# Optimization experiments

Measured on AMD Instinct MI355X. Metric: run time of the kernel, lower is better.

Reference implementation:

```python
import jax, jax.numpy as jnp
import numpy as np

B, N, F_IN, H, D = 16384, 64, 128, 4, 32


def setup_inputs() -> dict:
    key = jax.random.key(0)
    k1, k2, k3, k4, k5 = jax.random.split(key, 5)
    node_features = jax.random.normal(k1, (B, F_IN), dtype=jnp.float32)
    neighbor_features = jax.random.normal(k2, (B, N, F_IN), dtype=jnp.float32)
    mask = jax.random.randint(k3, (B, N), 0, 2).astype(jnp.bool_)
    # guarantee at least one valid neighbor per row (avoid all -inf softmax)
    neighbor_mask = mask.at[:, 0].set(True)
    # xavier_uniform with gain=1.414
    lim_W = 1.414 * np.sqrt(6.0 / (F_IN + H * D))
    W = jax.random.uniform(k4, (F_IN, H * D), minval=-lim_W, maxval=lim_W, dtype=jnp.float32)
    lim_a = 1.414 * np.sqrt(6.0 / (2 * D + 1))
    a = jax.random.uniform(k5, (H, 2 * D, 1), minval=-lim_a, maxval=lim_a, dtype=jnp.float32)
    return {"node_features": node_features, "neighbor_features": neighbor_features,
            "neighbor_mask": neighbor_mask, "W": W, "a": a}


def reference(node_features, neighbor_features, neighbor_mask, W, a):
    b, n, f_in = neighbor_features.shape
    h, two_d, _ = a.shape
    d = two_d // 2
    # project: (b,h,d) and (b,n,h,d)
    h_node = (node_features @ W).reshape(b, h, d)
    h_nb = (neighbor_features @ W).reshape(b, n, h, d)
    # concat-based additive attention: cat([h_node, h_nb]) @ a == h_node@a1 + h_nb@a2
    a1 = a[:, :d, 0]   # (h, d) node half
    a2 = a[:, d:, 0]   # (h, d) neighbor half
    e = (jnp.einsum('bhd,hd->bh', h_node, a1)[:, None, :]
         + jnp.einsum('bnhd,hd->bnh', h_nb, a2))          # (b, n, h)
    e = jax.nn.leaky_relu(e, negative_slope=0.2)
    e = jnp.where(neighbor_mask[:, :, None], e, -jnp.inf)
    alpha = jax.nn.softmax(e, axis=1)                      # softmax over neighbors
    # dropout is identity in eval mode
    out = jnp.einsum('bnh,bnhd->bhd', alpha, h_nb).reshape(b, h * d)
    return out
```

## Files before the change

### kernel.cpp

```cpp
#include <hip/hip_runtime.h>
#include <cstdint>


typedef __attribute__((ext_vector_type(8))) short bf16x8;
typedef __attribute__((ext_vector_type(4))) float f32x4;

union U16B { uint4 u; bf16x8 f; };

__device__ inline unsigned short f2bf(float x) {
  unsigned int u = __float_as_uint(x);
  unsigned int r = u + 0x7FFFu + ((u >> 16) & 1u);
  return (unsigned short)(r >> 16);
}

__global__ void gat_prep(const float* __restrict__ W, const float* __restrict__ a,
                         unsigned short* __restrict__ Wt, float* __restrict__ wa1) {
  int t = threadIdx.x;
  int blk = blockIdx.x;
  if (blk < 64) {
    int g = blk * 256 + t;
    int c = g >> 7, k = g & 127;
    Wt[c * 128 + k] = f2bf(W[k * 128 + c]);
  } else {
    for (int i = t; i < 512; i += 256) {
      int k = i >> 2, h = i & 3;
      float s = 0.f;
      #pragma unroll
      for (int d = 0; d < 32; ++d) s += W[k * 128 + h * 32 + d] * a[h * 64 + d];
      wa1[i] = s;
    }
  }
}

__global__ __launch_bounds__(256, 4) void gat_main(
    const float* __restrict__ node, const float* __restrict__ nbr,
    const unsigned char* __restrict__ mask, const unsigned short* __restrict__ Wt,
    const float* __restrict__ wa1, const float* __restrict__ a,
    float* __restrict__ out) {
  const int b    = blockIdx.x;
  const int tid  = threadIdx.x;
  const int w    = tid >> 6;
  const int lane = tid & 63;
  const int grp  = lane >> 4;
  const int l15  = lane & 15;

  __shared__ unsigned short Albs[64 * 128];

  unsigned int probe = ((const unsigned int*)mask)[lane];
  bool isByte = (__ballot(probe > 1u) != 0ull);

  bf16x8 bfr[2][4];
  #pragma unroll
  for (int j = 0; j < 2; ++j) {
    #pragma unroll
    for (int ks = 0; ks < 4; ++ks) {
      int c  = (2 * w + j) * 16 + l15;
      int k0 = grp * 8 + ks * 32;
      U16B u; u.u = *(const uint4*)(Wt + c * 128 + k0);
      bfr[j][ks] = u.f;
    }
  }

  float a2lo = a[w * 64 + 32 + l15];
  float a2hi = a[w * 64 + 48 + l15];

  float es = node[b * 128 + lane]      * wa1[lane * 4 + w]
           + node[b * 128 + 64 + lane] * wa1[(64 + lane) * 4 + w];
  #pragma unroll
  for (int m = 32; m >= 1; m >>= 1) es += __shfl_xor(es, m);

  unsigned int okm[4];
  if (isByte) {
    #pragma unroll
    for (int mt = 0; mt < 4; ++mt) {
      unsigned int mb = *(const unsigned int*)(mask + b * 64 + mt * 16 + grp * 4);
      okm[mt] = ((mb & 0xffu)       ? 1u : 0u) |
                ((mb & 0xff00u)     ? 2u : 0u) |
                ((mb & 0xff0000u)   ? 4u : 0u) |
                ((mb & 0xff000000u) ? 8u : 0u);
    }
  } else {
    const uint4* mi = (const uint4*)((const unsigned int*)mask + b * 64);
    #pragma unroll
    for (int mt = 0; mt < 4; ++mt) {
      uint4 mm = mi[mt * 4 + grp];
      okm[mt] = (mm.x ? 1u : 0u) | (mm.y ? 2u : 0u) | (mm.z ? 4u : 0u) | (mm.w ? 8u : 0u);
    }
  }

  {
    const float4* src = (const float4*)(nbr + (size_t)b * 8192);
    #pragma unroll
    for (int rep = 0; rep < 8; ++rep) {
      int v = rep * 256 + tid;
      float4 f = src[v];
      int r  = v >> 5;
      int kb = (v & 31) * 8;
      uint2 p;
      p.x = (unsigned int)f2bf(f.x) | ((unsigned int)f2bf(f.y) << 16);
      p.y = (unsigned int)f2bf(f.z) | ((unsigned int)f2bf(f.w) << 16);
      int byteaddr = (r * 256 + kb) ^ ((r & 7) << 4);
      *(uint2*)((char*)Albs + byteaddr) = p;
    }
  }
  __syncthreads();

  f32x4 acc[4][2];
  #pragma unroll
  for (int mt = 0; mt < 4; ++mt) { acc[mt][0] = f32x4{0,0,0,0}; acc[mt][1] = f32x4{0,0,0,0}; }
  #pragma unroll
  for (int mt = 0; mt < 4; ++mt) {
    #pragma unroll
    for (int ks = 0; ks < 4; ++ks) {
      int r     = mt * 16 + l15;
      int kbyte = (grp * 8 + ks * 32) * 2;
      int addr  = (r * 256 + kbyte) ^ ((r & 7) << 4);
      U16B u; u.u = *(const uint4*)((const char*)Albs + addr);
      acc[mt][0] = __builtin_amdgcn_mfma_f32_16x16x32_bf16(u.f, bfr[0][ks], acc[mt][0], 0, 0, 0);
      acc[mt][1] = __builtin_amdgcn_mfma_f32_16x16x32_bf16(u.f, bfr[1][ks], acc[mt][1], 0, 0, 0);
    }
  }

  float e[4][4];
  #pragma unroll
  for (int mt = 0; mt < 4; ++mt) {
    #pragma unroll
    for (int rg = 0; rg < 4; ++rg) {
      float v = acc[mt][0][rg] * a2lo + acc[mt][1][rg] * a2hi;
      v += __shfl_xor(v, 1); v += __shfl_xor(v, 2);
      v += __shfl_xor(v, 4); v += __shfl_xor(v, 8);
      float s = es + v;
      s = s > 0.f ? s : 0.2f * s;
      bool ok = (okm[mt] >> rg) & 1u;
      e[mt][rg] = ok ? s : -__builtin_inff();
    }
  }

  float M = -__builtin_inff();
  #pragma unroll
  for (int mt = 0; mt < 4; ++mt)
    #pragma unroll
    for (int rg = 0; rg < 4; ++rg) M = fmaxf(M, e[mt][rg]);
  M = fmaxf(M, __shfl_xor(M, 16));
  M = fmaxf(M, __shfl_xor(M, 32));

  float S = 0.f;
  float al[4][4];
  #pragma unroll
  for (int mt = 0; mt < 4; ++mt) {
    #pragma unroll
    for (int rg = 0; rg < 4; ++rg) {
      float p = __expf(e[mt][rg] - M);
      al[mt][rg] = p;
      S += p;
    }
  }
  S += __shfl_xor(S, 16);
  S += __shfl_xor(S, 32);
  float inv = 1.f / S;

  float po0 = 0.f, po1 = 0.f;
  #pragma unroll
  for (int mt = 0; mt < 4; ++mt) {
    #pragma unroll
    for (int rg = 0; rg < 4; ++rg) {
      po0 += al[mt][rg] * acc[mt][0][rg];
      po1 += al[mt][rg] * acc[mt][1][rg];
    }
  }
  po0 += __shfl_xor(po0, 16); po0 += __shfl_xor(po0, 32);
  po1 += __shfl_xor(po1, 16); po1 += __shfl_xor(po1, 32);
  po0 *= inv; po1 *= inv;

  if (lane < 32) {
    float vOut = (lane & 16) ? po1 : po0;
    out[b * 128 + w * 32 + lane] = vOut;
  }
}

extern "C" void kernel_launch(void* const* d_in, const int* in_sizes, int n_in,
                              void* d_out, int out_size, void* d_ws, size_t ws_size,
                              hipStream_t stream) {
  (void)in_sizes; (void)n_in; (void)out_size; (void)ws_size;
  const float* node = (const float*)d_in[0];
  const float* nbr  = (const float*)d_in[1];
  const unsigned char* mask = (const unsigned char*)d_in[2];
  const float* W    = (const float*)d_in[3];
  const float* a    = (const float*)d_in[4];
  float* out = (float*)d_out;

  unsigned short* Wt = (unsigned short*)d_ws;
  float* wa1 = (float*)((char*)d_ws + 32768);

  gat_prep<<<65, 256, 0, stream>>>(W, a, Wt, wa1);
  gat_main<<<16384, 256, 0, stream>>>(node, nbr, mask, Wt, wa1, a, out);
}
```

Baseline: 696.6 us.

## Process two batch rows per block with double-buffered LDS staging

Each block now handles two batch rows, so the block count is halved. The W fragment loads, a2 and wa1 loads are shared across both rows. The second row's neighbor tile is issued into registers before the first sync and written to a second LDS buffer while the first row is computed, overlapping global loads with MFMA work. LDS use per block doubles to 32 KB, register pressure rises from holding the 8 float4s, and launch bounds drop from 4 to 3 blocks per CU.

```diff
diff --git a/kernel.cpp b/kernel.cpp
--- a/kernel.cpp
+++ b/kernel.cpp
@@ -32,19 +32,97 @@
   }
 }
 
-__global__ __launch_bounds__(256, 4) void gat_main(
+__device__ __forceinline__ void compute_node(
+    const char* __restrict__ Abase, const bf16x8 (&bfr)[2][4],
+    float a2lo, float a2hi, float es, const unsigned int (&okm)[4],
+    int lane, int grp, int l15, int w, float* __restrict__ outp) {
+  f32x4 acc[4][2];
+  #pragma unroll
+  for (int mt = 0; mt < 4; ++mt) { acc[mt][0] = f32x4{0,0,0,0}; acc[mt][1] = f32x4{0,0,0,0}; }
+  #pragma unroll
+  for (int mt = 0; mt < 4; ++mt) {
+    #pragma unroll
+    for (int ks = 0; ks < 4; ++ks) {
+      int r     = mt * 16 + l15;
+      int kbyte = (grp * 8 + ks * 32) * 2;
+      int addr  = (r * 256 + kbyte) ^ ((r & 7) << 4);
+      U16B u; u.u = *(const uint4*)(Abase + addr);
+      acc[mt][0] = __builtin_amdgcn_mfma_f32_16x16x32_bf16(u.f, bfr[0][ks], acc[mt][0], 0, 0, 0);
+      acc[mt][1] = __builtin_amdgcn_mfma_f32_16x16x32_bf16(u.f, bfr[1][ks], acc[mt][1], 0, 0, 0);
+    }
+  }
+
+  float e[4][4];
+  #pragma unroll
+  for (int mt = 0; mt < 4; ++mt) {
+    #pragma unroll
+    for (int rg = 0; rg < 4; ++rg) {
+      float v = acc[mt][0][rg] * a2lo + acc[mt][1][rg] * a2hi;
+      v += __shfl_xor(v, 1); v += __shfl_xor(v, 2);
+      v += __shfl_xor(v, 4); v += __shfl_xor(v, 8);
+      float s = es + v;
+      s = s > 0.f ? s : 0.2f * s;
+      bool ok = (okm[mt] >> rg) & 1u;
+      e[mt][rg] = ok ? s : -__builtin_inff();
+    }
+  }
+
+  float M = -__builtin_inff();
+  #pragma unroll
+  for (int mt = 0; mt < 4; ++mt)
+    #pragma unroll
+    for (int rg = 0; rg < 4; ++rg) M = fmaxf(M, e[mt][rg]);
+  M = fmaxf(M, __shfl_xor(M, 16));
+  M = fmaxf(M, __shfl_xor(M, 32));
+
+  float S = 0.f;
+  float al[4][4];
+  #pragma unroll
+  for (int mt = 0; mt < 4; ++mt) {
+    #pragma unroll
+    for (int rg = 0; rg < 4; ++rg) {
+      float p = __expf(e[mt][rg] - M);
+      al[mt][rg] = p;
+      S += p;
+    }
+  }
+  S += __shfl_xor(S, 16);
+  S += __shfl_xor(S, 32);
+  float inv = 1.f / S;
+
+  float po0 = 0.f, po1 = 0.f;
+  #pragma unroll
+  for (int mt = 0; mt < 4; ++mt) {
+    #pragma unroll
+    for (int rg = 0; rg < 4; ++rg) {
+      po0 += al[mt][rg] * acc[mt][0][rg];
+      po1 += al[mt][rg] * acc[mt][1][rg];
+    }
+  }
+  po0 += __shfl_xor(po0, 16); po0 += __shfl_xor(po0, 32);
+  po1 += __shfl_xor(po1, 16); po1 += __shfl_xor(po1, 32);
+  po0 *= inv; po1 *= inv;
+
+  if (lane < 32) {
+    float vOut = (lane & 16) ? po1 : po0;
+    outp[w * 32 + lane] = vOut;
+  }
+}
+
+__global__ __launch_bounds__(256, 3) void gat_main(
     const float* __restrict__ node, const float* __restrict__ nbr,
     const unsigned char* __restrict__ mask, const unsigned short* __restrict__ Wt,
     const float* __restrict__ wa1, const float* __restrict__ a,
     float* __restrict__ out) {
-  const int b    = blockIdx.x;
+  const int b0   = blockIdx.x * 2;
+  const int b1   = b0 + 1;
   const int tid  = threadIdx.x;
   const int w    = tid >> 6;
   const int lane = tid & 63;
   const int grp  = lane >> 4;
   const int l15  = lane & 15;
 
-  __shared__ unsigned short Albs[64 * 128];
+  __shared__ unsigned short Albs[2][64 * 128];
 
   unsigned int probe = ((const unsigned int*)mask)[lane];
   bool isByte = (__ballot(probe > 1u) != 0ull);
@@ -64,32 +142,39 @@
   float a2lo = a[w * 64 + 32 + l15];
   float a2hi = a[w * 64 + 48 + l15];
 
-  float es = node[b * 128 + lane]      * wa1[lane * 4 + w]
-           + node[b * 128 + 64 + lane] * wa1[(64 + lane) * 4 + w];
-  #pragma unroll
-  for (int m = 32; m >= 1; m >>= 1) es += __shfl_xor(es, m);
-
-  unsigned int okm[4];
+  float wv0 = wa1[lane * 4 + w];
+  float wv1 = wa1[(64 + lane) * 4 + w];
+  float es0 = node[b0 * 128 + lane] * wv0 + node[b0 * 128 + 64 + lane] * wv1;
+  float es1 = node[b1 * 128 + lane] * wv0 + node[b1 * 128 + 64 + lane] * wv1;
+  #pragma unroll
+  for (int m = 32; m >= 1; m >>= 1) { es0 += __shfl_xor(es0, m); es1 += __shfl_xor(es1, m); }
+
+  unsigned int okm0[4], okm1[4];
   if (isByte) {
     #pragma unroll
     for (int mt = 0; mt < 4; ++mt) {
-      unsigned int mb = *(const unsigned int*)(mask + b * 64 + mt * 16 + grp * 4);
-      okm[mt] = ((mb & 0xffu)       ? 1u : 0u) |
-                ((mb & 0xff00u)     ? 2u : 0u) |
-                ((mb & 0xff0000u)   ? 4u : 0u) |
-                ((mb & 0xff000000u) ? 8u : 0u);
+      unsigned int m0 = *(const unsigned int*)(mask + b0 * 64 + mt * 16 + grp * 4);
+      unsigned int m1 = *(const unsigned int*)(mask + b1 * 64 + mt * 16 + grp * 4);
+      okm0[mt] = ((m0 & 0xffu) ? 1u : 0u) | ((m0 & 0xff00u) ? 2u : 0u) |
+                 ((m0 & 0xff0000u) ? 4u : 0u) | ((m0 & 0xff000000u) ? 8u : 0u);
+      okm1[mt] = ((m1 & 0xffu) ? 1u : 0u) | ((m1 & 0xff00u) ? 2u : 0u) |
+                 ((m1 & 0xff0000u) ? 4u : 0u) | ((m1 & 0xff000000u) ? 8u : 0u);
     }
   } else {
-    const uint4* mi = (const uint4*)((const unsigned int*)mask + b * 64);
+    const uint4* mi0 = (const uint4*)((const unsigned int*)mask + b0 * 64);
+    const uint4* mi1 = (const uint4*)((const unsigned int*)mask + b1 * 64);
     #pragma unroll
     for (int mt = 0; mt < 4; ++mt) {
-      uint4 mm = mi[mt * 4 + grp];
-      okm[mt] = (mm.x ? 1u : 0u) | (mm.y ? 2u : 0u) | (mm.z ? 4u : 0u) | (mm.w ? 8u : 0u);
+      uint4 q0 = mi0[mt * 4 + grp];
+      uint4 q1 = mi1[mt * 4 + grp];
+      okm0[mt] = (q0.x ? 1u : 0u) | (q0.y ? 2u : 0u) | (q0.z ? 4u : 0u) | (q0.w ? 8u : 0u);
+      okm1[mt] = (q1.x ? 1u : 0u) | (q1.y ? 2u : 0u) | (q1.z ? 4u : 0u) | (q1.w ? 8u : 0u);
     }
   }
 
   {
-    const float4* src = (const float4*)(nbr + (size_t)b * 8192);
+    const float4* src = (const float4*)(nbr + (size_t)b0 * 8192);
+    char* base = (char*)&Albs[0][0];
     #pragma unroll
     for (int rep = 0; rep < 8; ++rep) {
       int v = rep * 256 + tid;
@@ -100,82 +185,42 @@
       p.x = (unsigned int)f2bf(f.x) | ((unsigned int)f2bf(f.y) << 16);
       p.y = (unsigned int)f2bf(f.z) | ((unsigned int)f2bf(f.w) << 16);
       int byteaddr = (r * 256 + kb) ^ ((r & 7) << 4);
-      *(uint2*)((char*)Albs + byteaddr) = p;
-    }
-  }
+      *(uint2*)(base + byteaddr) = p;
+    }
+  }
+
+  float4 s1[8];
+  {
+    const float4* src = (const float4*)(nbr + (size_t)b1 * 8192);
+    #pragma unroll
+    for (int rep = 0; rep < 8; ++rep) s1[rep] = src[rep * 256 + tid];
+  }
+
   __syncthreads();
 
-  f32x4 acc[4][2];
-  #pragma unroll
-  for (int mt = 0; mt < 4; ++mt) { acc[mt][0] = f32x4{0,0,0,0}; acc[mt][1] = f32x4{0,0,0,0}; }
-  #pragma unroll
-  for (int mt = 0; mt < 4; ++mt) {
-    #pragma unroll
-    for (int ks = 0; ks < 4; ++ks) {
-      int r     = mt * 16 + l15;
-      int kbyte = (grp * 8 + ks * 32) * 2;
-      int addr  = (r * 256 + kbyte) ^ ((r & 7) << 4);
-      U16B u; u.u = *(const uint4*)((const char*)Albs + addr);
-      acc[mt][0] = __builtin_amdgcn_mfma_f32_16x16x32_bf16(u.f, bfr[0][ks], acc[mt][0], 0, 0, 0);
-      acc[mt][1] = __builtin_amdgcn_mfma_f32_16x16x32_bf16(u.f, bfr[1][ks], acc[mt][1], 0, 0, 0);
-    }
-  }
-
-  float e[4][4];
-  #pragma unroll
-  for (int mt = 0; mt < 4; ++mt) {
-    #pragma unroll
-    for (int rg = 0; rg < 4; ++rg) {
-      float v = acc[mt][0][rg] * a2lo + acc[mt][1][rg] * a2hi;
-      v += __shfl_xor(v, 1); v += __shfl_xor(v, 2);
-      v += __shfl_xor(v, 4); v += __shfl_xor(v, 8);
-      float s = es + v;
-      s = s > 0.f ? s : 0.2f * s;
-      bool ok = (okm[mt] >> rg) & 1u;
-      e[mt][rg] = ok ? s : -__builtin_inff();
-    }
-  }
-
-  float M = -__builtin_inff();
-  #pragma unroll
-  for (int mt = 0; mt < 4; ++mt)
-    #pragma unroll
-    for (int rg = 0; rg < 4; ++rg) M = fmaxf(M, e[mt][rg]);
-  M = fmaxf(M, __shfl_xor(M, 16));
-  M = fmaxf(M, __shfl_xor(M, 32));
-
-  float S = 0.f;
-  float al[4][4];
-  #pragma unroll
-  for (int mt = 0; mt < 4; ++mt) {
-    #pragma unroll
-    for (int rg = 0; rg < 4; ++rg) {
-      float p = __expf(e[mt][rg] - M);
-      al[mt][rg] = p;
-      S += p;
-    }
-  }
-  S += __shfl_xor(S, 16);
-  S += __shfl_xor(S, 32);
-  float inv = 1.f / S;
-
-  float po0 = 0.f, po1 = 0.f;
-  #pragma unroll
-  for (int mt = 0; mt < 4; ++mt) {
-    #pragma unroll
-    for (int rg = 0; rg < 4; ++rg) {
-      po0 += al[mt][rg] * acc[mt][0][rg];
-      po1 += al[mt][rg] * acc[mt][1][rg];
-    }
-  }
-  po0 += __shfl_xor(po0, 16); po0 += __shfl_xor(po0, 32);
-  po1 += __shfl_xor(po1, 16); po1 += __shfl_xor(po1, 32);
-  po0 *= inv; po1 *= inv;
-
-  if (lane < 32) {
-    float vOut = (lane & 16) ? po1 : po0;
-    out[b * 128 + w * 32 + lane] = vOut;
-  }
+  {
+    char* base = (char*)&Albs[1][0];
+    #pragma unroll
+    for (int rep = 0; rep < 8; ++rep) {
+      int v = rep * 256 + tid;
+      float4 f = s1[rep];
+      int r  = v >> 5;
+      int kb = (v & 31) * 8;
+      uint2 p;
+      p.x = (unsigned int)f2bf(f.x) | ((unsigned int)f2bf(f.y) << 16);
+      p.y = (unsigned int)f2bf(f.z) | ((unsigned int)f2bf(f.w) << 16);
+      int byteaddr = (r * 256 + kb) ^ ((r & 7) << 4);
+      *(uint2*)(base + byteaddr) = p;
+    }
+  }
+
+  compute_node((const char*)&Albs[0][0], bfr, a2lo, a2hi, es0, okm0,
+               lane, grp, l15, w, out + (size_t)b0 * 128);
+
+  __syncthreads();
+
+  compute_node((const char*)&Albs[1][0], bfr, a2lo, a2hi, es1, okm1,
+               lane, grp, l15, w, out + (size_t)b1 * 128);
 }
 
 extern "C" void kernel_launch(void* const* d_in, const int* in_sizes, int n_in,
@@ -193,5 +238,5 @@
   float* wa1 = (float*)((char*)d_ws + 32768);
 
   gat_prep<<<65, 256, 0, stream>>>(W, a, Wt, wa1);
-  gat_main<<<16384, 256, 0, stream>>>(node, nbr, mask, Wt, wa1, a, out);
-}
+  gat_main<<<8192, 256, 0, stream>>>(node, nbr, mask, Wt, wa1, a, out);
+}
```

Result: slower. 732.6 us (+5.2%).
